# Optimization experiments

Measured on AMD Instinct MI355X. Metric: run time of the kernel, lower is better.

The kernel has to match this reference:

```python
import jax, jax.numpy as jnp
import numpy as np

B, T, C = 2, 2048, 2048
N_HEAD = 16
HEAD_DIM = C // N_HEAD


def setup_inputs() -> dict:
    key = jax.random.key(0)
    ks = jax.random.split(key, 5)
    s = 1.0 / np.sqrt(C)
    return {
        "x": jax.random.normal(ks[0], (B, T, C), dtype=jnp.float32),
        "Wq": jax.random.normal(ks[1], (C, C), dtype=jnp.float32) * s,
        "bq": jnp.zeros((C,), dtype=jnp.float32),
        "Wk": jax.random.normal(ks[2], (C, C), dtype=jnp.float32) * s,
        "bk": jnp.zeros((C,), dtype=jnp.float32),
        "Wv": jax.random.normal(ks[3], (C, C), dtype=jnp.float32) * s,
        "bv": jnp.zeros((C,), dtype=jnp.float32),
        "Wp": jax.random.normal(ks[4], (C, C), dtype=jnp.float32) * s,
        "bp": jnp.zeros((C,), dtype=jnp.float32),
    }


def reference(x, Wq, bq, Wk, bk, Wv, bv, Wp, bp):
    Bx, Tx, Cx = x.shape
    # torch nn.Linear: y = x @ W.T + b
    def lin(x, W, b):
        return jnp.einsum("btc,dc->btd", x, W) + b

    def split_heads(y):  # (B,T,C) -> (B,H,T,hd)
        return y.reshape(Bx, Tx, N_HEAD, HEAD_DIM).transpose(0, 2, 1, 3)

    q = split_heads(lin(x, Wq, bq))
    k = split_heads(lin(x, Wk, bk))
    v = split_heads(lin(x, Wv, bv))

    scale = 1.0 / np.sqrt(HEAD_DIM).astype(np.float32)
    attn = jnp.einsum("bhqd,bhkd->bhqk", q, k) * scale  # (B,H,T,T)
    causal = jnp.tril(jnp.ones((Tx, Tx), dtype=bool))
    attn = jnp.where(causal[None, None], attn, -jnp.inf)
    attn = jax.nn.softmax(attn, axis=-1)
    out = jnp.einsum("bhqk,bhkd->bhqd", attn, v)  # (B,H,T,hd)
    # Faithful to original: transpose(-2,-1) swaps T and head_dim, then
    # a contiguous view reinterprets memory as (B,T,C).
    out = out.transpose(0, 1, 3, 2).reshape(Bx, Tx, Cx)
    return lin(out, Wp, bp)
```

## Files before the change

### kernel.cpp

```cpp
#include <hip/hip_runtime.h>
#include <stdint.h>

#define DEVI __device__ __forceinline__

typedef __attribute__((ext_vector_type(8))) short short8;
typedef __attribute__((ext_vector_type(4))) float f32x4;
typedef __attribute__((ext_vector_type(4))) unsigned int u32x4;

static constexpr int Bn = 2;
static constexpr int Tn = 2048;
static constexpr int Cn = 2048;
static constexpr int NH = 16;
static constexpr int HD = 128;
static constexpr int Kdim = 2048;

DEVI unsigned short f2bf(float f) {
  union { float f; unsigned u; } v; v.f = f;
  return (unsigned short)((v.u + 0x7FFFu + ((v.u >> 16) & 1u)) >> 16);
}

DEVI void gload_lds16(const void* g, void* l) {
  __builtin_amdgcn_global_load_lds(
      (const __attribute__((address_space(1))) void*)g,
      (__attribute__((address_space(3))) void*)l, 16, 0, 0);
}

__global__ __launch_bounds__(256) void cast_bf16_kernel(
    const float* __restrict__ src, unsigned short* __restrict__ dst, int n) {
  int idx = (blockIdx.x * blockDim.x + threadIdx.x) * 4;
  const int stride = gridDim.x * blockDim.x * 4;
  for (; idx < n; idx += stride) {
    f32x4 f = *(const f32x4*)(src + idx);
    unsigned short o[4];
    o[0] = f2bf(f[0]); o[1] = f2bf(f[1]); o[2] = f2bf(f[2]); o[3] = f2bf(f[3]);
    *(unsigned long long*)(dst + idx) = *(const unsigned long long*)o;
  }
}

__global__ __launch_bounds__(256) void cast4_kernel(
    const float* __restrict__ s0, const float* __restrict__ s1,
    const float* __restrict__ s2, const float* __restrict__ s3,
    unsigned short* __restrict__ d0, unsigned short* __restrict__ d1,
    unsigned short* __restrict__ d2, unsigned short* __restrict__ d3, int n) {
  const int w = blockIdx.y;
  const float* src = (w == 0) ? s0 : (w == 1) ? s1 : (w == 2) ? s2 : s3;
  unsigned short* dst = (w == 0) ? d0 : (w == 1) ? d1 : (w == 2) ? d2 : d3;
  int idx = (blockIdx.x * blockDim.x + threadIdx.x) * 4;
  const int stride = gridDim.x * blockDim.x * 4;
  for (; idx < n; idx += stride) {
    f32x4 f = *(const f32x4*)(src + idx);
    unsigned short o[4];
    o[0] = f2bf(f[0]); o[1] = f2bf(f[1]); o[2] = f2bf(f[2]); o[3] = f2bf(f[3]);
    *(unsigned long long*)(dst + idx) = *(const unsigned long long*)o;
  }
}

#define G_BAR() __builtin_amdgcn_s_barrier()
#define G_MFMA(d, a, b) d = __builtin_amdgcn_mfma_f32_16x16x32_bf16(a, b, d, 0, 0, 0)

__global__ __launch_bounds__(512, 2) void gemm_qkv_256x192_kernel(
    const unsigned short* __restrict__ X,
    const unsigned short* __restrict__ W3,
    const float* __restrict__ bq_, const float* __restrict__ bk_, const float* __restrict__ bv_,
    unsigned short* __restrict__ Qo, unsigned short* __restrict__ Ko,
    unsigned short* __restrict__ Vo) {
  constexpr int NT = Kdim / 64;
  __shared__ unsigned short L[2][28672];

  const int tid = threadIdx.x;
  const int wave = tid >> 6, lane = tid & 63;
  const int wm = wave >> 2, wn = wave & 3;
  const int quad = lane >> 4, lr = lane & 15;

  const int flat = (int)blockIdx.x + 32 * (int)blockIdx.y;
  const int swz = (flat & 7) * 64 + (flat >> 3);
  const int bx = swz & 31, by = swz >> 5;
  const int n0 = bx * 192;
  const int m0 = by * 256;

  f32x4 acc[8][3];
  const f32x4 zero4 = {0.f, 0.f, 0.f, 0.f};
#pragma unroll
  for (int i = 0; i < 8; ++i)
#pragma unroll
    for (int j = 0; j < 3; ++j) acc[i][j] = zero4;

  const int srow = tid >> 3;
  const int schunk = (tid & 7) ^ (srow & 7);
  const unsigned short* Asrc = X + (size_t)(m0 + srow) * Kdim + schunk * 8;
  const unsigned short* Bsrc = W3 + (size_t)(n0 + srow) * Kdim + schunk * 8;

  auto STAGE_A = [&](int buf, int t) {
    unsigned short* d = &L[buf][tid * 8];
    const unsigned short* s = Asrc + t * 64;
#pragma unroll
    for (int h = 0; h < 4; ++h)
      gload_lds16(s + (size_t)(h * 64) * Kdim, d + h * 4096);
  };
  auto STAGE_B = [&](int buf, int t) {
    unsigned short* d = &L[buf][16384 + tid * 8];
    const unsigned short* s = Bsrc + t * 64;
#pragma unroll
    for (int h = 0; h < 3; ++h)
      gload_lds16(s + (size_t)(h * 64) * Kdim, d + h * 4096);
  };

  const int pc0 = quad ^ (lr & 7);
  const int pc1 = (4 + quad) ^ (lr & 7);
  const int aoff = (wm * 128 + lr) * 64;
  const int boff = 16384 + (wn * 48 + lr) * 64;

  STAGE_A(0, 0);
  STAGE_B(0, 0);
  STAGE_B(1, 1);
  asm volatile("s_waitcnt vmcnt(3)" ::: "memory");
  G_BAR();

  short8 Af[4][2], Bf[3][2];

  for (int t = 0; t < NT; ++t) {
    const int cur = t & 1, nxt = cur ^ 1;
#pragma unroll
    for (int m = 0; m < 4; ++m) {
      Af[m][0] = *(const short8*)&L[cur][aoff + m * 1024 + pc0 * 8];
      Af[m][1] = *(const short8*)&L[cur][aoff + m * 1024 + pc1 * 8];
    }
#pragma unroll
    for (int n = 0; n < 3; ++n) {
      Bf[n][0] = *(const short8*)&L[cur][boff + n * 1024 + pc0 * 8];
      Bf[n][1] = *(const short8*)&L[cur][boff + n * 1024 + pc1 * 8];
    }
    if (t + 1 < NT) STAGE_A(nxt, t + 1);
    G_BAR();
    __builtin_amdgcn_s_setprio(1);
#pragma unroll
    for (int m = 0; m < 4; ++m)
#pragma unroll
      for (int n = 0; n < 3; ++n) {
        G_MFMA(acc[m][n], Af[m][0], Bf[n][0]);
        G_MFMA(acc[m][n], Af[m][1], Bf[n][1]);
      }
    __builtin_amdgcn_s_setprio(0);
    G_BAR();
#pragma unroll
    for (int m = 0; m < 4; ++m) {
      Af[m][0] = *(const short8*)&L[cur][aoff + (m + 4) * 1024 + pc0 * 8];
      Af[m][1] = *(const short8*)&L[cur][aoff + (m + 4) * 1024 + pc1 * 8];
    }
    if (t + 2 < NT) STAGE_B(cur, t + 2);
    G_BAR();
    __builtin_amdgcn_s_setprio(1);
#pragma unroll
    for (int m = 0; m < 4; ++m)
#pragma unroll
      for (int n = 0; n < 3; ++n) {
        G_MFMA(acc[m + 4][n], Af[m][0], Bf[n][0]);
        G_MFMA(acc[m + 4][n], Af[m][1], Bf[n][1]);
      }
    __builtin_amdgcn_s_setprio(0);
    if (t < NT - 2) { asm volatile("s_waitcnt vmcnt(3)" ::: "memory"); }
    else            { asm volatile("s_waitcnt vmcnt(0)" ::: "memory"); }
    G_BAR();
  }

#pragma unroll
  for (int ni = 0; ni < 3; ++ni) {
    const int n = n0 + wn * 48 + ni * 16 + lr;
    const int mat = n >> 11;
    const int nl = n & 2047;
    const int h = nl >> 7, d = nl & 127;
    const float bv = (mat == 0 ? bq_ : mat == 1 ? bk_ : bv_)[nl];
    if (mat == 2) {
#pragma unroll
      for (int mi = 0; mi < 8; ++mi) {
        const int m = m0 + wm * 128 + mi * 16 + quad * 4;
        const int b = m >> 11, tt = m & 2047;
        unsigned short o4[4];
#pragma unroll
        for (int r = 0; r < 4; ++r) o4[r] = f2bf(acc[mi][ni][r] + bv);
        *(unsigned long long*)&Vo[(((size_t)(b * NH + h)) * HD + d) * Tn + tt] =
            *(const unsigned long long*)o4;
      }
    } else {
      unsigned short* Out = (mat == 0) ? Qo : Ko;
#pragma unroll
      for (int mi = 0; mi < 8; ++mi) {
#pragma unroll
        for (int r = 0; r < 4; ++r) {
          const int m = m0 + wm * 128 + mi * 16 + quad * 4 + r;
          const int b = m >> 11, tt = m & 2047;
          Out[(((size_t)(b * NH + h)) * Tn + tt) * HD + d] = f2bf(acc[mi][ni][r] + bv);
        }
      }
    }
  }
}

__global__ __launch_bounds__(512, 2) void gemm_proj_256x128_kernel(
    const unsigned short* __restrict__ Aall,
    const unsigned short* __restrict__ Wp_,
    const float* __restrict__ bias,
    float* __restrict__ Y) {
  constexpr int NT = Kdim / 64;
  __shared__ unsigned short L[2][24576];

  const int tid = threadIdx.x;
  const int wave = tid >> 6, lane = tid & 63;
  const int wm = wave >> 2, wn = wave & 3;
  const int quad = lane >> 4, lr = lane & 15;

  const int flat = (int)blockIdx.x + 16 * (int)blockIdx.y;
  const int swz = (flat & 7) * 16 + (flat >> 3);
  const int bx = swz % 16, by = swz / 16;
  const int m0 = by * 256, n0 = bx * 128;
  const int bz = blockIdx.z;
  const unsigned short* A = Aall + (size_t)bz * Cn * Tn;

  f32x4 acc[8][2];
  const f32x4 zero4 = {0.f, 0.f, 0.f, 0.f};
#pragma unroll
  for (int i = 0; i < 8; ++i)
#pragma unroll
    for (int j = 0; j < 2; ++j) acc[i][j] = zero4;

  const int srow = tid >> 3;
  const int schunk = (tid & 7) ^ (srow & 7);
  const unsigned short* Asrc = A + (size_t)(m0 + srow) * Kdim + schunk * 8;
  const unsigned short* Bsrc = Wp_ + (size_t)(n0 + srow) * Kdim + schunk * 8;

  auto STAGE_A = [&](int buf, int h, int t) {
    unsigned short* d = &L[buf][h * 8192 + tid * 8];
    const unsigned short* s = Asrc + (size_t)(h * 128) * Kdim + t * 64;
    gload_lds16(s, d);
    gload_lds16(s + (size_t)64 * Kdim, d + 4096);
  };
  auto STAGE_B = [&](int buf, int t) {
    unsigned short* d = &L[buf][16384 + tid * 8];
    const unsigned short* s = Bsrc + t * 64;
    gload_lds16(s, d);
    gload_lds16(s + (size_t)64 * Kdim, d + 4096);
  };

  const int pc0 = quad ^ (lr & 7);
  const int pc1 = (4 + quad) ^ (lr & 7);
  const int aoff = (wm * 128 + lr) * 64;
  const int boff = 16384 + (wn * 32 + lr) * 64;

  STAGE_A(0, 0, 0); STAGE_A(0, 1, 0);
  STAGE_B(0, 0);
  STAGE_B(1, 1);
  asm volatile("s_waitcnt vmcnt(2)" ::: "memory");
  G_BAR();

  short8 Af[4][2], Bf[2][2];

  for (int t = 0; t < NT; ++t) {
    const int cur = t & 1, nxt = cur ^ 1;
#pragma unroll
    for (int m = 0; m < 4; ++m) {
      Af[m][0] = *(const short8*)&L[cur][aoff + m * 1024 + pc0 * 8];
      Af[m][1] = *(const short8*)&L[cur][aoff + m * 1024 + pc1 * 8];
    }
#pragma unroll
    for (int n = 0; n < 2; ++n) {
      Bf[n][0] = *(const short8*)&L[cur][boff + n * 1024 + pc0 * 8];
      Bf[n][1] = *(const short8*)&L[cur][boff + n * 1024 + pc1 * 8];
    }
    if (t + 1 < NT) STAGE_A(nxt, 0, t + 1);
    G_BAR();
    __builtin_amdgcn_s_setprio(1);
#pragma unroll
    for (int m = 0; m < 4; ++m)
#pragma unroll
      for (int n = 0; n < 2; ++n) {
        G_MFMA(acc[m][n], Af[m][0], Bf[n][0]);
        G_MFMA(acc[m][n], Af[m][1], Bf[n][1]);
      }
    __builtin_amdgcn_s_setprio(0);
    G_BAR();
#pragma unroll
    for (int m = 0; m < 4; ++m) {
      Af[m][0] = *(const short8*)&L[cur][aoff + (m + 4) * 1024 + pc0 * 8];
      Af[m][1] = *(const short8*)&L[cur][aoff + (m + 4) * 1024 + pc1 * 8];
    }
    if (t + 1 < NT) STAGE_A(nxt, 1, t + 1);
    if (t + 2 < NT) STAGE_B(cur, t + 2);
    G_BAR();
    __builtin_amdgcn_s_setprio(1);
#pragma unroll
    for (int m = 0; m < 4; ++m)
#pragma unroll
      for (int n = 0; n < 2; ++n) {
        G_MFMA(acc[m + 4][n], Af[m][0], Bf[n][0]);
        G_MFMA(acc[m + 4][n], Af[m][1], Bf[n][1]);
      }
    __builtin_amdgcn_s_setprio(0);
    if (t < NT - 2) { asm volatile("s_waitcnt vmcnt(2)" ::: "memory"); }
    else            { asm volatile("s_waitcnt vmcnt(0)" ::: "memory"); }
    G_BAR();
  }

#pragma unroll
  for (int ni = 0; ni < 2; ++ni) {
    const int n = n0 + wn * 32 + ni * 16 + lr;
    const float bv = bias[n];
#pragma unroll
    for (int mi = 0; mi < 8; ++mi) {
#pragma unroll
      for (int r = 0; r < 4; ++r) {
        const int m = m0 + wm * 128 + mi * 16 + quad * 4 + r;
        Y[((size_t)bz * Tn + m) * Cn + n] = acc[mi][ni][r] + bv;
      }
    }
  }
}

__global__ __launch_bounds__(512, 2) void attn_kernel(
    const unsigned short* __restrict__ Q,
    const unsigned short* __restrict__ K,
    const unsigned short* __restrict__ V,
    unsigned short* __restrict__ Ot) {
  constexpr int KST = 136;
  constexpr int VST = 136;
  constexpr int PST = 136;
  __shared__ unsigned short SMEM[54400];
  unsigned short* Ks = SMEM;
  unsigned short* Vs = SMEM + 17408;
  unsigned short* Ps = SMEM + 36992;

  const int tid = threadIdx.x;
  const int wave = tid >> 6, lane = tid & 63;
  const int wb = wave & 3;
  const int wh = wave >> 2;
  const int quad = lane >> 4, lr = lane & 15;
  const int bh = blockIdx.y;
  const float SL = 0.08838834764831845f * 1.4426950408889634f;

  const unsigned short* Kp = K + (size_t)bh * Tn * HD;
  const unsigned short* Vp = V + (size_t)bh * HD * Tn;
  unsigned short* Pw = &Ps[wb * 32 * PST];

  const int r = tid >> 2;
  const int cc = (tid & 3) * 32;
  unsigned short* kl = &Ks[r * KST + cc];
  unsigned short* vl = &Vs[r * VST + cc];
  u32x4 kreg[4], vreg[4];

  const f32x4 zero4 = {0.f, 0.f, 0.f, 0.f};
#pragma unroll 1
  for (int half = 0; half < 2; ++half) {
    const int jt = half ? (15 - (int)blockIdx.x) : (int)blockIdx.x;
    const int q0 = jt * 128;

    for (int i = tid; i < 16 * VST; i += 512) Vs[128 * VST + i] = 0x3F80;

    const unsigned short* Qp = Q + ((size_t)bh * Tn + q0 + wb * 32) * HD;
    short8 qf[2][4];
#pragma unroll
    for (int mi = 0; mi < 2; ++mi)
#pragma unroll
      for (int ks = 0; ks < 4; ++ks)
        qf[mi][ks] = *(const short8*)&Qp[(mi * 16 + lr) * HD + ks * 32 + quad * 8];

    f32x4 oacc[2][9];
#pragma unroll
    for (int mi = 0; mi < 2; ++mi)
#pragma unroll
      for (int nd = 0; nd < 9; ++nd) oacc[mi][nd] = zero4;

    const int nch = q0 / 128 + 1;

    {
      const unsigned short* kg = &Kp[(size_t)r * HD + cc];
      const unsigned short* vg = &Vp[(size_t)r * Tn + cc];
#pragma unroll
      for (int p = 0; p < 4; ++p) {
        kreg[p] = *(const u32x4*)(kg + p * 8);
        vreg[p] = *(const u32x4*)(vg + p * 8);
      }
    }

    for (int c = 0; c < nch; ++c) {
      const int k0 = c * 128;
#pragma unroll
      for (int p = 0; p < 4; ++p) {
        *(u32x4*)(kl + p * 8) = kreg[p];
        *(u32x4*)(vl + p * 8) = vreg[p];
      }
      __syncthreads();
      if (c + 1 < nch) {
        const int k1 = k0 + 128;
        const unsigned short* kg = &Kp[(size_t)(k1 + r) * HD + cc];
        const unsigned short* vg = &Vp[(size_t)r * Tn + k1 + cc];
#pragma unroll
        for (int p = 0; p < 4; ++p) {
          kreg[p] = *(const u32x4*)(kg + p * 8);
          vreg[p] = *(const u32x4*)(vg + p * 8);
        }
      }

      f32x4 sa[2][4];
#pragma unroll
      for (int mi = 0; mi < 2; ++mi)
#pragma unroll
        for (int n4 = 0; n4 < 4; ++n4) sa[mi][n4] = zero4;
#pragma unroll
      for (int n4 = 0; n4 < 4; ++n4) {
        const int nt = wh * 4 + n4;
        short8 kf[4];
#pragma unroll
        for (int ks = 0; ks < 4; ++ks)
          kf[ks] = *(const short8*)&Ks[(nt * 16 + lr) * KST + ks * 32 + quad * 8];
#pragma unroll
        for (int mi = 0; mi < 2; ++mi)
#pragma unroll
          for (int ks = 0; ks < 4; ++ks)
            sa[mi][n4] = __builtin_amdgcn_mfma_f32_16x16x32_bf16(qf[mi][ks], kf[ks], sa[mi][n4], 0, 0, 0);
      }

      if (k0 == q0) {
#pragma unroll
        for (int mi = 0; mi < 2; ++mi)
#pragma unroll
          for (int n4 = 0; n4 < 4; ++n4)
#pragma unroll
            for (int r2 = 0; r2 < 4; ++r2) {
              const int qg = q0 + wb * 32 + mi * 16 + quad * 4 + r2;
              const int kg = k0 + (wh * 4 + n4) * 16 + lr;
              if (kg > qg) sa[mi][n4][r2] = -3.0e38f;
            }
      }

#pragma unroll
      for (int mi = 0; mi < 2; ++mi)
#pragma unroll
        for (int n4 = 0; n4 < 4; ++n4)
#pragma unroll
          for (int r2 = 0; r2 < 4; ++r2) {
            const float p = __builtin_amdgcn_exp2f(sa[mi][n4][r2] * SL);
            Pw[(mi * 16 + quad * 4 + r2) * PST + (wh * 4 + n4) * 16 + lr] = f2bf(p);
          }

#pragma unroll
      for (int k2 = 0; k2 < 2; ++k2) {
        const int kt = wh * 2 + k2;
        short8 pf[2];
#pragma unroll
        for (int mi = 0; mi < 2; ++mi)
          pf[mi] = *(const short8*)&Pw[(mi * 16 + lr) * PST + kt * 32 + quad * 8];
#pragma unroll
        for (int nd = 0; nd < 9; ++nd) {
          short8 vf = *(const short8*)&Vs[(nd * 16 + lr) * VST + kt * 32 + quad * 8];
#pragma unroll
          for (int mi = 0; mi < 2; ++mi)
            oacc[mi][nd] = __builtin_amdgcn_mfma_f32_16x16x32_bf16(pf[mi], vf, oacc[mi][nd], 0, 0, 0);
        }
      }
      __syncthreads();
    }

    f32x4* cbuf = (f32x4*)SMEM;
    if (wh == 1) {
#pragma unroll
      for (int mi = 0; mi < 2; ++mi)
#pragma unroll
        for (int nd = 0; nd < 9; ++nd)
          cbuf[(wb * 64 + lane) * 18 + mi * 9 + nd] = oacc[mi][nd];
    }
    __syncthreads();
    if (wh == 0) {
#pragma unroll
      for (int mi = 0; mi < 2; ++mi)
#pragma unroll
        for (int nd = 0; nd < 9; ++nd)
          oacc[mi][nd] += cbuf[(wb * 64 + lane) * 18 + mi * 9 + nd];
#pragma unroll
      for (int mi = 0; mi < 2; ++mi)
#pragma unroll
        for (int r2 = 0; r2 < 4; ++r2) {
          const float rl = 1.0f / oacc[mi][8][r2];
          const int tl = wb * 32 + mi * 16 + quad * 4 + r2;
#pragma unroll
          for (int nd = 0; nd < 8; ++nd)
            Ps[tl * PST + nd * 16 + lr] = f2bf(oacc[mi][nd][r2] * rl);
        }
    }
    __syncthreads();
    if (tid < 256) {
      unsigned short* Od = Ot + (size_t)bh * HD * Tn + q0;
#pragma unroll
      for (int p = 0; p < 8; ++p) {
        const int d = p * 16 + (tid >> 4);
        const int t8 = (tid & 15) * 8;
        alignas(16) unsigned short v[8];
#pragma unroll
        for (int j = 0; j < 8; ++j) v[j] = Ps[(t8 + j) * PST + d];
        *(u32x4*)&Od[(size_t)d * Tn + t8] = *(const u32x4*)v;
      }
    }
    __syncthreads();
  }
}

extern "C" void kernel_launch(void* const* d_in, const int* in_sizes, int n_in,
                              void* d_out, int out_size, void* d_ws, size_t ws_size,
                              hipStream_t stream) {
  const float* x  = (const float*)d_in[0];
  const float* Wq = (const float*)d_in[1];
  const float* bq = (const float*)d_in[2];
  const float* Wk = (const float*)d_in[3];
  const float* bk = (const float*)d_in[4];
  const float* Wv = (const float*)d_in[5];
  const float* bv = (const float*)d_in[6];
  const float* Wp = (const float*)d_in[7];
  const float* bp = (const float*)d_in[8];
  float* out = (float*)d_out;

  char* ws = (char*)d_ws;
  const size_t MB = 1ull << 20;
  unsigned short* Xbf = (unsigned short*)(ws);
  unsigned short* Wqb = (unsigned short*)(ws + 16 * MB);
  unsigned short* Wkb = (unsigned short*)(ws + 24 * MB);
  unsigned short* Wvb = (unsigned short*)(ws + 32 * MB);
  unsigned short* Wpb = (unsigned short*)(ws + 40 * MB);
  unsigned short* Qb  = (unsigned short*)(ws + 48 * MB);
  unsigned short* Kb  = (unsigned short*)(ws + 64 * MB);
  unsigned short* Vtb = (unsigned short*)(ws + 80 * MB);
  unsigned short* Otb = (unsigned short*)(ws + 96 * MB);

  cast_bf16_kernel<<<dim3(1024), dim3(256), 0, stream>>>(x, Xbf, Bn * Tn * Cn);
  cast4_kernel<<<dim3(512, 4), dim3(256), 0, stream>>>(
      Wq, Wk, Wv, Wp, Wqb, Wkb, Wvb, Wpb, Cn * Cn);

  gemm_qkv_256x192_kernel<<<dim3(32, 16), dim3(512), 0, stream>>>(
      Xbf, Wqb , bq, bk, bv, Qb, Kb, Vtb);

  attn_kernel<<<dim3(8, Bn * NH), dim3(512), 0, stream>>>(Qb, Kb, Vtb, Otb);

  gemm_proj_256x128_kernel<<<dim3(16, 8, 2), dim3(512), 0, stream>>>(
      Otb, Wpb, bp, out);
}
```

Before: 373.2 us.

## Split QKV GEMM k-loop into four phases with finer-grained async staging

After: 370.1 us. Within noise of the previous version (-0.8%).

```diff
diff --git a/kernel.cpp b/kernel.cpp
--- a/kernel.cpp
+++ b/kernel.cpp
@@ -90,78 +90,94 @@
   const unsigned short* Asrc = X + (size_t)(m0 + srow) * Kdim + schunk * 8;
   const unsigned short* Bsrc = W3 + (size_t)(n0 + srow) * Kdim + schunk * 8;
 
-  auto STAGE_A = [&](int buf, int t) {
-    unsigned short* d = &L[buf][tid * 8];
-    const unsigned short* s = Asrc + t * 64;
-#pragma unroll
-    for (int h = 0; h < 4; ++h)
-      gload_lds16(s + (size_t)(h * 64) * Kdim, d + h * 4096);
+  auto STAGE_A2 = [&](int buf, int h, int t) {
+    unsigned short* d = &L[buf][h * 8192 + tid * 8];
+    const unsigned short* s = Asrc + (size_t)(h * 128) * Kdim + t * 64;
+    gload_lds16(s, d);
+    gload_lds16(s + (size_t)64 * Kdim, d + 4096);
   };
-  auto STAGE_B = [&](int buf, int t) {
+  auto STAGE_B2 = [&](int buf, int t) {
     unsigned short* d = &L[buf][16384 + tid * 8];
     const unsigned short* s = Bsrc + t * 64;
-#pragma unroll
-    for (int h = 0; h < 3; ++h)
-      gload_lds16(s + (size_t)(h * 64) * Kdim, d + h * 4096);
+    gload_lds16(s, d);
+    gload_lds16(s + (size_t)64 * Kdim, d + 4096);
+  };
+  auto STAGE_B1 = [&](int buf, int t) {
+    unsigned short* d = &L[buf][16384 + 8192 + tid * 8];
+    const unsigned short* s = Bsrc + (size_t)128 * Kdim + t * 64;
+    gload_lds16(s, d);
   };
 
   const int pc0 = quad ^ (lr & 7);
   const int pc1 = (4 + quad) ^ (lr & 7);
   const int aoff = (wm * 128 + lr) * 64;
   const int boff = 16384 + (wn * 48 + lr) * 64;
-
-  STAGE_A(0, 0);
-  STAGE_B(0, 0);
-  STAGE_B(1, 1);
+#define RDA(mi, pc) (*(const short8*)&L[cur][aoff + (mi) * 1024 + (pc) * 8])
+#define RDB(ni, pc) (*(const short8*)&L[cur][boff + (ni) * 1024 + (pc) * 8])
+
+  STAGE_A2(0, 0, 0); STAGE_A2(0, 1, 0);
+  STAGE_B2(0, 0); STAGE_B1(0, 0);
+  STAGE_B2(1, 1); STAGE_B1(1, 1);
   asm volatile("s_waitcnt vmcnt(3)" ::: "memory");
   G_BAR();
 
-  short8 Af[4][2], Bf[3][2];
+  short8 Af[4], Bf[3][2];
 
   for (int t = 0; t < NT; ++t) {
     const int cur = t & 1, nxt = cur ^ 1;
 #pragma unroll
-    for (int m = 0; m < 4; ++m) {
-      Af[m][0] = *(const short8*)&L[cur][aoff + m * 1024 + pc0 * 8];
-      Af[m][1] = *(const short8*)&L[cur][aoff + m * 1024 + pc1 * 8];
-    }
-#pragma unroll
-    for (int n = 0; n < 3; ++n) {
-      Bf[n][0] = *(const short8*)&L[cur][boff + n * 1024 + pc0 * 8];
-      Bf[n][1] = *(const short8*)&L[cur][boff + n * 1024 + pc1 * 8];
-    }
-    if (t + 1 < NT) STAGE_A(nxt, t + 1);
+    for (int m = 0; m < 4; ++m) Af[m] = RDA(m, pc0);
+#pragma unroll
+    for (int n = 0; n < 3; ++n) Bf[n][0] = RDB(n, pc0);
+    if (t + 1 < NT) STAGE_A2(nxt, 0, t + 1);
     G_BAR();
     __builtin_amdgcn_s_setprio(1);
 #pragma unroll
     for (int m = 0; m < 4; ++m)
 #pragma unroll
-      for (int n = 0; n < 3; ++n) {
-        G_MFMA(acc[m][n], Af[m][0], Bf[n][0]);
-        G_MFMA(acc[m][n], Af[m][1], Bf[n][1]);
-      }
+      for (int n = 0; n < 3; ++n) G_MFMA(acc[m][n], Af[m], Bf[n][0]);
     __builtin_amdgcn_s_setprio(0);
     G_BAR();
 #pragma unroll
-    for (int m = 0; m < 4; ++m) {
-      Af[m][0] = *(const short8*)&L[cur][aoff + (m + 4) * 1024 + pc0 * 8];
-      Af[m][1] = *(const short8*)&L[cur][aoff + (m + 4) * 1024 + pc1 * 8];
-    }
-    if (t + 2 < NT) STAGE_B(cur, t + 2);
+    for (int m = 0; m < 4; ++m) Af[m] = RDA(m, pc1);
+#pragma unroll
+    for (int n = 0; n < 3; ++n) Bf[n][1] = RDB(n, pc1);
+    if (t + 1 < NT) STAGE_A2(nxt, 1, t + 1);
     G_BAR();
     __builtin_amdgcn_s_setprio(1);
 #pragma unroll
     for (int m = 0; m < 4; ++m)
 #pragma unroll
-      for (int n = 0; n < 3; ++n) {
-        G_MFMA(acc[m + 4][n], Af[m][0], Bf[n][0]);
-        G_MFMA(acc[m + 4][n], Af[m][1], Bf[n][1]);
-      }
+      for (int n = 0; n < 3; ++n) G_MFMA(acc[m][n], Af[m], Bf[n][1]);
+    __builtin_amdgcn_s_setprio(0);
+    G_BAR();
+#pragma unroll
+    for (int m = 0; m < 4; ++m) Af[m] = RDA(m + 4, pc0);
+    if (t + 2 < NT) STAGE_B2(cur, t + 2);
+    G_BAR();
+    __builtin_amdgcn_s_setprio(1);
+#pragma unroll
+    for (int m = 0; m < 4; ++m)
+#pragma unroll
+      for (int n = 0; n < 3; ++n) G_MFMA(acc[m + 4][n], Af[m], Bf[n][0]);
+    __builtin_amdgcn_s_setprio(0);
+    G_BAR();
+#pragma unroll
+    for (int m = 0; m < 4; ++m) Af[m] = RDA(m + 4, pc1);
+    if (t + 2 < NT) STAGE_B1(cur, t + 2);
+    G_BAR();
+    __builtin_amdgcn_s_setprio(1);
+#pragma unroll
+    for (int m = 0; m < 4; ++m)
+#pragma unroll
+      for (int n = 0; n < 3; ++n) G_MFMA(acc[m + 4][n], Af[m], Bf[n][1]);
     __builtin_amdgcn_s_setprio(0);
     if (t < NT - 2) { asm volatile("s_waitcnt vmcnt(3)" ::: "memory"); }
     else            { asm volatile("s_waitcnt vmcnt(0)" ::: "memory"); }
     G_BAR();
   }
+#undef RDA
+#undef RDB
 
 #pragma unroll
   for (int ni = 0; ni < 3; ++ni) {
```

## Switch QKV GEMM to 32x32x16 MFMA with 256x384 tiles and K=32 stages

Applied to the files above, without the earlier changes.

New measurement: 370.7 us. About the same (-0.7%).

```diff
diff --git a/kernel.cpp b/kernel.cpp
--- a/kernel.cpp
+++ b/kernel.cpp
@@ -5,6 +5,7 @@
 
 typedef __attribute__((ext_vector_type(8))) short short8;
 typedef __attribute__((ext_vector_type(4))) float f32x4;
+typedef __attribute__((ext_vector_type(16))) float f32x16;
 typedef __attribute__((ext_vector_type(4))) unsigned int u32x4;
 
 static constexpr int Bn = 2;
@@ -57,139 +58,135 @@
 
 #define G_BAR() __builtin_amdgcn_s_barrier()
 #define G_MFMA(d, a, b) d = __builtin_amdgcn_mfma_f32_16x16x32_bf16(a, b, d, 0, 0, 0)
-
-__global__ __launch_bounds__(512, 2) void gemm_qkv_256x192_kernel(
+#define G_MFMA32(d, a, b) d = __builtin_amdgcn_mfma_f32_32x32x16_bf16(a, b, d, 0, 0, 0)
+
+__global__ __launch_bounds__(512, 2) void gemm_qkv_32x32_kernel(
     const unsigned short* __restrict__ X,
     const unsigned short* __restrict__ W3,
     const float* __restrict__ bq_, const float* __restrict__ bk_, const float* __restrict__ bv_,
     unsigned short* __restrict__ Qo, unsigned short* __restrict__ Ko,
     unsigned short* __restrict__ Vo) {
-  constexpr int NT = Kdim / 64;
-  __shared__ unsigned short L[2][28672];
+  constexpr int NT = Kdim / 32;
+  __shared__ unsigned short L[2][20480];
 
   const int tid = threadIdx.x;
   const int wave = tid >> 6, lane = tid & 63;
   const int wm = wave >> 2, wn = wave & 3;
-  const int quad = lane >> 4, lr = lane & 15;
-
-  const int flat = (int)blockIdx.x + 32 * (int)blockIdx.y;
-  const int swz = (flat & 7) * 64 + (flat >> 3);
-  const int bx = swz & 31, by = swz >> 5;
-  const int n0 = bx * 192;
+  const int l31 = lane & 31, hi = lane >> 5;
+
+  const int flat = (int)blockIdx.x + 16 * (int)blockIdx.y;
+  const int swz = (flat & 7) * 32 + (flat >> 3);
+  const int bx = swz & 15, by = swz >> 4;
+  const int n0 = bx * 384;
   const int m0 = by * 256;
 
-  f32x4 acc[8][3];
-  const f32x4 zero4 = {0.f, 0.f, 0.f, 0.f};
-#pragma unroll
-  for (int i = 0; i < 8; ++i)
-#pragma unroll
-    for (int j = 0; j < 3; ++j) acc[i][j] = zero4;
-
-  const int srow = tid >> 3;
-  const int schunk = (tid & 7) ^ (srow & 7);
+  f32x16 acc[4][3];
+  {
+    f32x16 z;
+#pragma unroll
+    for (int k = 0; k < 16; ++k) z[k] = 0.f;
+#pragma unroll
+    for (int i = 0; i < 4; ++i)
+#pragma unroll
+      for (int j = 0; j < 3; ++j) acc[i][j] = z;
+  }
+
+  const int srow = tid >> 2;
+  const int schunk = (tid & 3) ^ ((tid >> 2) & 3) ^ ((tid >> 4) & 3);
   const unsigned short* Asrc = X + (size_t)(m0 + srow) * Kdim + schunk * 8;
   const unsigned short* Bsrc = W3 + (size_t)(n0 + srow) * Kdim + schunk * 8;
 
-  auto STAGE_A = [&](int buf, int t) {
-    unsigned short* d = &L[buf][tid * 8];
-    const unsigned short* s = Asrc + t * 64;
-#pragma unroll
-    for (int h = 0; h < 4; ++h)
-      gload_lds16(s + (size_t)(h * 64) * Kdim, d + h * 4096);
+  auto STAGE_A = [&](int buf, int h, int t) {
+    gload_lds16(Asrc + (size_t)(h * 128) * Kdim + t * 32,
+                &L[buf][h * 4096 + tid * 8]);
   };
-  auto STAGE_B = [&](int buf, int t) {
-    unsigned short* d = &L[buf][16384 + tid * 8];
-    const unsigned short* s = Bsrc + t * 64;
-#pragma unroll
-    for (int h = 0; h < 3; ++h)
-      gload_lds16(s + (size_t)(h * 64) * Kdim, d + h * 4096);
+  auto STAGE_B = [&](int buf, int h, int t) {
+    gload_lds16(Bsrc + (size_t)(h * 128) * Kdim + t * 32,
+                &L[buf][8192 + h * 4096 + tid * 8]);
   };
 
-  const int pc0 = quad ^ (lr & 7);
-  const int pc1 = (4 + quad) ^ (lr & 7);
-  const int aoff = (wm * 128 + lr) * 64;
-  const int boff = 16384 + (wn * 48 + lr) * 64;
-
-  STAGE_A(0, 0);
-  STAGE_B(0, 0);
-  STAGE_B(1, 1);
+  const int xorv = (lane & 3) ^ ((lane >> 2) & 3);
+  const int pc0 = ((0 + hi) ^ xorv) * 8;
+  const int pc1 = ((2 + hi) ^ xorv) * 8;
+  const int arow = (wm * 128 + l31) * 32;
+  const int brow = 8192 + (wn * 96 + l31) * 32;
+#define RDA(mi, pc) (*(const short8*)&L[cur][arow + (mi) * 1024 + (pc)])
+#define RDB(ni, pc) (*(const short8*)&L[cur][brow + (ni) * 1024 + (pc)])
+
+  STAGE_A(0, 0, 0); STAGE_A(0, 1, 0);
+  STAGE_B(0, 0, 0); STAGE_B(0, 1, 0); STAGE_B(0, 2, 0);
+  STAGE_B(1, 0, 1); STAGE_B(1, 1, 1); STAGE_B(1, 2, 1);
   asm volatile("s_waitcnt vmcnt(3)" ::: "memory");
   G_BAR();
 
-  short8 Af[4][2], Bf[3][2];
+  short8 Af[4], Bf[3][2];
 
   for (int t = 0; t < NT; ++t) {
     const int cur = t & 1, nxt = cur ^ 1;
 #pragma unroll
-    for (int m = 0; m < 4; ++m) {
-      Af[m][0] = *(const short8*)&L[cur][aoff + m * 1024 + pc0 * 8];
-      Af[m][1] = *(const short8*)&L[cur][aoff + m * 1024 + pc1 * 8];
-    }
-#pragma unroll
-    for (int n = 0; n < 3; ++n) {
-      Bf[n][0] = *(const short8*)&L[cur][boff + n * 1024 + pc0 * 8];
-      Bf[n][1] = *(const short8*)&L[cur][boff + n * 1024 + pc1 * 8];
-    }
-    if (t + 1 < NT) STAGE_A(nxt, t + 1);
+    for (int m = 0; m < 4; ++m) Af[m] = RDA(m, pc0);
+#pragma unroll
+    for (int n = 0; n < 3; ++n) { Bf[n][0] = RDB(n, pc0); Bf[n][1] = RDB(n, pc1); }
+    if (t + 1 < NT) { STAGE_A(nxt, 0, t + 1); STAGE_A(nxt, 1, t + 1); }
     G_BAR();
     __builtin_amdgcn_s_setprio(1);
 #pragma unroll
     for (int m = 0; m < 4; ++m)
 #pragma unroll
-      for (int n = 0; n < 3; ++n) {
-        G_MFMA(acc[m][n], Af[m][0], Bf[n][0]);
-        G_MFMA(acc[m][n], Af[m][1], Bf[n][1]);
-      }
+      for (int n = 0; n < 3; ++n) G_MFMA32(acc[m][n], Af[m], Bf[n][0]);
     __builtin_amdgcn_s_setprio(0);
     G_BAR();
 #pragma unroll
-    for (int m = 0; m < 4; ++m) {
-      Af[m][0] = *(const short8*)&L[cur][aoff + (m + 4) * 1024 + pc0 * 8];
-      Af[m][1] = *(const short8*)&L[cur][aoff + (m + 4) * 1024 + pc1 * 8];
-    }
-    if (t + 2 < NT) STAGE_B(cur, t + 2);
+    for (int m = 0; m < 4; ++m) Af[m] = RDA(m, pc1);
+    if (t + 2 < NT) { STAGE_B(cur, 0, t + 2); STAGE_B(cur, 1, t + 2); STAGE_B(cur, 2, t + 2); }
     G_BAR();
     __builtin_amdgcn_s_setprio(1);
 #pragma unroll
     for (int m = 0; m < 4; ++m)
 #pragma unroll
-      for (int n = 0; n < 3; ++n) {
-        G_MFMA(acc[m + 4][n], Af[m][0], Bf[n][0]);
-        G_MFMA(acc[m + 4][n], Af[m][1], Bf[n][1]);
-      }
+      for (int n = 0; n < 3; ++n) G_MFMA32(acc[m][n], Af[m], Bf[n][1]);
     __builtin_amdgcn_s_setprio(0);
     if (t < NT - 2) { asm volatile("s_waitcnt vmcnt(3)" ::: "memory"); }
     else            { asm volatile("s_waitcnt vmcnt(0)" ::: "memory"); }
     G_BAR();
   }
+#undef RDA
+#undef RDB
 
 #pragma unroll
   for (int ni = 0; ni < 3; ++ni) {
-    const int n = n0 + wn * 48 + ni * 16 + lr;
+    const int n = n0 + wn * 96 + ni * 32 + l31;
     const int mat = n >> 11;
     const int nl = n & 2047;
     const int h = nl >> 7, d = nl & 127;
     const float bv = (mat == 0 ? bq_ : mat == 1 ? bk_ : bv_)[nl];
     if (mat == 2) {
 #pragma unroll
-      for (int mi = 0; mi < 8; ++mi) {
-        const int m = m0 + wm * 128 + mi * 16 + quad * 4;
-        const int b = m >> 11, tt = m & 2047;
-        unsigned short o4[4];
-#pragma unroll
-        for (int r = 0; r < 4; ++r) o4[r] = f2bf(acc[mi][ni][r] + bv);
-        *(unsigned long long*)&Vo[(((size_t)(b * NH + h)) * HD + d) * Tn + tt] =
-            *(const unsigned long long*)o4;
+      for (int mi = 0; mi < 4; ++mi) {
+#pragma unroll
+        for (int rq = 0; rq < 4; ++rq) {
+          const int m = m0 + wm * 128 + mi * 32 + rq * 8 + hi * 4;
+          const int b = m >> 11, tt = m & 2047;
+          unsigned short o4[4];
+#pragma unroll
+          for (int r = 0; r < 4; ++r) o4[r] = f2bf(acc[mi][ni][rq * 4 + r] + bv);
+          *(unsigned long long*)&Vo[(((size_t)(b * NH + h)) * HD + d) * Tn + tt] =
+              *(const unsigned long long*)o4;
+        }
       }
     } else {
       unsigned short* Out = (mat == 0) ? Qo : Ko;
 #pragma unroll
-      for (int mi = 0; mi < 8; ++mi) {
-#pragma unroll
-        for (int r = 0; r < 4; ++r) {
-          const int m = m0 + wm * 128 + mi * 16 + quad * 4 + r;
-          const int b = m >> 11, tt = m & 2047;
-          Out[(((size_t)(b * NH + h)) * Tn + tt) * HD + d] = f2bf(acc[mi][ni][r] + bv);
+      for (int mi = 0; mi < 4; ++mi) {
+#pragma unroll
+        for (int rq = 0; rq < 4; ++rq) {
+#pragma unroll
+          for (int r = 0; r < 4; ++r) {
+            const int m = m0 + wm * 128 + mi * 32 + rq * 8 + hi * 4 + r;
+            const int b = m >> 11, tt = m & 2047;
+            Out[(((size_t)(b * NH + h)) * Tn + tt) * HD + d] =
+                f2bf(acc[mi][ni][rq * 4 + r] + bv);
+          }
         }
       }
     }
@@ -532,7 +529,7 @@
   cast4_kernel<<<dim3(512, 4), dim3(256), 0, stream>>>(
       Wq, Wk, Wv, Wp, Wqb, Wkb, Wvb, Wpb, Cn * Cn);
 
-  gemm_qkv_256x192_kernel<<<dim3(32, 16), dim3(512), 0, stream>>>(
+  gemm_qkv_32x32_kernel<<<dim3(16, 16), dim3(512), 0, stream>>>(
       Xbf, Wqb , bq, bk, bv, Qb, Kb, Vtb);
 
   attn_kernel<<<dim3(8, Bn * NH), dim3(512), 0, stream>>>(Qb, Kb, Vtb, Otb);
```
